# Performance work log

Measured on AMD Instinct MI355X. Metric: run time of the kernel, lower is better.

The kernel has to match this reference:

```python
import jax, jax.numpy as jnp
import numpy as np

EMB = 1024
HEADS = 16
HEAD_DIM = EMB // HEADS


def setup_inputs() -> dict:
    key = jax.random.key(0)
    ks = jax.random.split(key, 9)
    s = 1.0 / np.sqrt(EMB)
    x = jax.random.normal(ks[0], (2, 2048, EMB), dtype=jnp.float32)
    Wq = jax.random.normal(ks[1], (EMB, EMB), dtype=jnp.float32) * s
    bq = jnp.zeros((EMB,), dtype=jnp.float32)
    Wk = jax.random.normal(ks[2], (EMB, EMB), dtype=jnp.float32) * s
    bk = jnp.zeros((EMB,), dtype=jnp.float32)
    Wv = jax.random.normal(ks[3], (EMB, EMB), dtype=jnp.float32) * s
    bv = jnp.zeros((EMB,), dtype=jnp.float32)
    Wo = jax.random.normal(ks[4], (EMB, EMB), dtype=jnp.float32) * s
    bo = jnp.zeros((EMB,), dtype=jnp.float32)
    return {"x": x, "Wq": Wq, "bq": bq, "Wk": Wk, "bk": bk,
            "Wv": Wv, "bv": bv, "Wo": Wo, "bo": bo}


def reference(x, Wq, bq, Wk, bk, Wv, bv, Wo, bo):
    B, S, E = x.shape
    # torch Linear: y = x @ W.T + b
    q = x @ Wq.T + bq
    k = x @ Wk.T + bk
    v = x @ Wv.T + bv
    # [B,S,E] -> [B,H,S,D]
    q = q.reshape(B, S, HEADS, HEAD_DIM).transpose(0, 2, 1, 3)
    k = k.reshape(B, S, HEADS, HEAD_DIM).transpose(0, 2, 1, 3)
    v = v.reshape(B, S, HEADS, HEAD_DIM).transpose(0, 2, 1, 3)
    energy = jnp.einsum('bhqd,bhkd->bhqk', q, k)
    scaling = jnp.float32(E) ** 0.5  # NOTE: sqrt(emb_size), not sqrt(head_dim), as in source
    att = jax.nn.softmax(energy / scaling, axis=-1)
    out = jnp.einsum('bhqk,bhkd->bhqd', att, v)
    out = out.transpose(0, 2, 1, 3).reshape(B, S, E)
    return out @ Wo.T + bo
```

## Files before the change

kernel.cpp:

```cpp
#include <hip/hip_runtime.h>
#include <stdint.h>


typedef _Float16 half8  __attribute__((ext_vector_type(8)));
typedef _Float16 half4v __attribute__((ext_vector_type(4)));
typedef float    f32x4  __attribute__((ext_vector_type(4)));
typedef float    f32x16 __attribute__((ext_vector_type(16)));

#define GLD16(g, l) __builtin_amdgcn_global_load_lds(                         \
    (__attribute__((address_space(1))) void*)(g),                            \
    (__attribute__((address_space(3))) void*)(l), 16, 0, 0)

#define MFMA16(a, b, c) __builtin_amdgcn_mfma_f32_16x16x32_f16((a), (b), (c), 0, 0, 0)
#define MFMA32(a, b, c) __builtin_amdgcn_mfma_f32_32x32x16_f16((a), (b), (c), 0, 0, 0)

#if __has_builtin(__builtin_amdgcn_exp2f)
#define EXP2(x) __builtin_amdgcn_exp2f(x)
#else
#define EXP2(x) exp2f(x)
#endif

static __device__ inline uint32_t pk_u32(float a, float b)
{
    auto t = __builtin_amdgcn_cvt_pkrtz(a, b);
    return __builtin_bit_cast(uint32_t, t);
}

__global__ void cvt_all(const float* __restrict__ x,  const float* __restrict__ wq,
                        const float* __restrict__ wk, const float* __restrict__ wv,
                        const float* __restrict__ wo, _Float16* __restrict__ xb,
                        _Float16* __restrict__ wqkv, _Float16* __restrict__ wob)
{
    int i = blockIdx.x * blockDim.x + threadIdx.x;
    const float* src; _Float16* dst; int off;
    if (i < 1048576)      { src = x;  dst = xb;                 off = i; }
    else if (i < 1310720) { src = wq; dst = wqkv;               off = i - 1048576; }
    else if (i < 1572864) { src = wk; dst = wqkv + 1048576;     off = i - 1310720; }
    else if (i < 1835008) { src = wv; dst = wqkv + 2097152;     off = i - 1572864; }
    else                  { src = wo; dst = wob;                off = i - 1835008; }
    float4 f = ((const float4*)src)[off];
    half4v h = { (_Float16)f.x, (_Float16)f.y, (_Float16)f.z, (_Float16)f.w };
    ((half4v*)dst)[off] = h;
}

template<int BN, int MODE>
__global__ __launch_bounds__(256, MODE == 0 ? 3 : 2)
void gemm_f16(const _Float16* __restrict__ A, const _Float16* __restrict__ W,
              const float* __restrict__ b0, const float* __restrict__ b1,
              const float* __restrict__ b2, _Float16* __restrict__ o0,
              _Float16* __restrict__ o1, _Float16* __restrict__ o2,
              float* __restrict__ outf, float qscale)
{
    constexpr int NI = BN / 32;
    __shared__ _Float16 lA[128 * 64];
    __shared__ _Float16 lB[BN * 64];
    const int m0 = blockIdx.y * 128, n0 = blockIdx.x * BN;
    const int tid = threadIdx.x, lane = tid & 63, w = tid >> 6;
    const int wr = (w >> 1) * 64, wc = (w & 1) * (BN / 2);
    const int lrow = lane & 15, lk4 = lane >> 4;
    f32x4 acc[4][NI] = {};

    for (int k0 = 0; k0 < 1024; k0 += 64) {
        __syncthreads();
#pragma unroll
        for (int c = 0; c < 4; ++c) {
            int sidx = c * 256 + tid;
            int row = sidx >> 3, sl = sidx & 7;
            int gc = k0 + ((sl ^ (row & 7)) << 3);
            GLD16(A + (size_t)(m0 + row) * 1024 + gc, lA + (size_t)(c * 256 + w * 64) * 8);
        }
#pragma unroll
        for (int c = 0; c < BN / 32; ++c) {
            int sidx = c * 256 + tid;
            int row = sidx >> 3, sl = sidx & 7;
            int gc = k0 + ((sl ^ (row & 7)) << 3);
            GLD16(W + (size_t)(n0 + row) * 1024 + gc, lB + (size_t)(c * 256 + w * 64) * 8);
        }
        __syncthreads();

#pragma unroll
        for (int kd = 0; kd < 2; ++kd) {
            half8 af[4], bf[NI];
#pragma unroll
            for (int mi = 0; mi < 4; ++mi) {
                int ra = wr + mi * 16 + lrow;
                af[mi] = *(const half8*)(lA + ra * 64 + (((kd * 4 + lk4) ^ (ra & 7)) * 8));
            }
#pragma unroll
            for (int ni = 0; ni < NI; ++ni) {
                int rb = wc + ni * 16 + lrow;
                bf[ni] = *(const half8*)(lB + rb * 64 + (((kd * 4 + lk4) ^ (rb & 7)) * 8));
            }
#pragma unroll
            for (int mi = 0; mi < 4; ++mi)
#pragma unroll
                for (int ni = 0; ni < NI; ++ni)
                    acc[mi][ni] = MFMA16(af[mi], bf[ni], acc[mi][ni]);
        }
    }

    if (MODE == 0) {
        const int which = n0 >> 10;
        const float* bp = which == 0 ? b0 : which == 1 ? b1 : b2;
        const float scale = which == 0 ? qscale : 1.f;
        const int nh = n0 & 1023;
        float bcol[NI];
#pragma unroll
        for (int ni = 0; ni < NI; ++ni) bcol[ni] = bp[nh + wc + ni * 16 + lrow];
        if (which == 2) {
#pragma unroll
            for (int mi = 0; mi < 4; ++mi)
#pragma unroll
                for (int ni = 0; ni < NI; ++ni) {
                    int cg = nh + wc + ni * 16 + lrow;
                    int hh = cg >> 6, dd = cg & 63;
                    int sb = m0 + wr + mi * 16 + lk4 * 4;
                    int bb = sb >> 11, ss = sb & 2047;
                    int tile = ss >> 6, ks = (ss >> 4) & 3;
                    int hb = (ss >> 3) & 1, j0 = ss & 7;
                    int c2 = dd >> 5, l31v = dd & 31;
                    half4v pkv;
#pragma unroll
                    for (int r = 0; r < 4; ++r)
                        pkv[r] = (_Float16)(acc[mi][ni][r] + bcol[ni]);
                    size_t off = (size_t)(bb * 16 + hh) * 131072
                               + tile * 4096 + (ks * 2 + c2) * 512
                               + hb * 256 + l31v * 8 + j0;
                    *(half4v*)(o2 + off) = pkv;
                }
        } else if (which == 1) {
#pragma unroll
            for (int mi = 0; mi < 4; ++mi)
#pragma unroll
                for (int ni = 0; ni < NI; ++ni)
#pragma unroll
                    for (int r = 0; r < 4; ++r) {
                        int rg = m0 + wr + mi * 16 + lk4 * 4 + r;
                        int cg = nh + wc + ni * 16 + lrow;
                        float v = acc[mi][ni][r] + bcol[ni];
                        int bb = rg >> 11, ss = rg & 2047;
                        int hh = cg >> 6, dd = cg & 63;
                        int tile = ss >> 6, sbl = (ss >> 5) & 1, l31v = ss & 31;
                        int kd = dd >> 4, hv = (dd >> 3) & 1, jv = dd & 7;
                        size_t off = (size_t)(bb * 16 + hh) * 131072
                                   + tile * 4096 + (sbl * 4 + kd) * 512
                                   + hv * 256 + l31v * 8 + jv;
                        o1[off] = (_Float16)v;
                    }
        } else {
            _Float16* outh = o0;
#pragma unroll
            for (int mi = 0; mi < 4; ++mi)
#pragma unroll
                for (int ni = 0; ni < NI; ++ni)
#pragma unroll
                    for (int r = 0; r < 4; ++r) {
                        int rg = m0 + wr + mi * 16 + lk4 * 4 + r;
                        int cg = nh + wc + ni * 16 + lrow;
                        float v = (acc[mi][ni][r] + bcol[ni]) * scale;
                        int b = rg >> 11, s = rg & 2047, hh = cg >> 6, dd = cg & 63;
                        outh[(((size_t)b * 16 + hh) * 2048 + s) * 64 + dd] = (_Float16)v;
                    }
        }
    } else {
        float bcol[NI];
#pragma unroll
        for (int ni = 0; ni < NI; ++ni) bcol[ni] = b0[n0 + wc + ni * 16 + lrow];
#pragma unroll
        for (int mi = 0; mi < 4; ++mi)
#pragma unroll
            for (int ni = 0; ni < NI; ++ni)
#pragma unroll
                for (int r = 0; r < 4; ++r) {
                    int rg = m0 + wr + mi * 16 + lk4 * 4 + r;
                    int cg = n0 + wc + ni * 16 + lrow;
                    outf[(size_t)rg * 1024 + cg] = acc[mi][ni][r] + bcol[ni];
                }
    }
}

#define KVB 64
#define NT  32
__global__ __launch_bounds__(256, 2)
void attn(const _Float16* __restrict__ q, const _Float16* __restrict__ kf_,
          const _Float16* __restrict__ vf_, _Float16* __restrict__ ao)
{
    __shared__ _Float16 lKV[3 * 8192];
    const int bid0 = blockIdx.x;
    const int bid = (bid0 & 7) * 64 + (bid0 >> 3);
    const int bh = bid >> 4, q0 = (bid & 15) * 128;
    const int bb = bh >> 4, hh = bh & 15;
    const int tid = threadIdx.x, lane = tid & 63, w = tid >> 6;
    const int l31 = lane & 31, h = lane >> 5;
    const _Float16* qh = q + (size_t)bh * 2048 * 64;
    const _Float16* khf = kf_ + (size_t)bh * 131072;
    const _Float16* vhf = vf_ + (size_t)bh * 131072;

    half8 qf[4];
#pragma unroll
    for (int kd = 0; kd < 4; ++kd)
        qf[kd] = *(const half8*)(qh + (size_t)(q0 + w * 32 + l31) * 64
                                    + kd * 16 + h * 8);

    float l_ = 0.f;
    f32x16 o0 = {}, o1 = {};
    f32x16 eA0 = {}, eA1 = {}, eB0 = {}, eB1 = {};

    int sv = 0, sk = 1, sw = 2;

    auto STAGE = [&](int t, int bs) {
        const _Float16* ks = khf + (size_t)t * 4096;
        const _Float16* vs = vhf + (size_t)t * 4096;
        _Float16* dst = lKV + bs * 8192;
#pragma unroll
        for (int c = 0; c < 2; ++c) {
            int p = c * 256 + tid;
            GLD16(ks + (size_t)p * 8, dst + (size_t)p * 8);
            GLD16(vs + (size_t)p * 8, dst + 4096 + (size_t)p * 8);
        }
    };

    auto SOFTMAX = [&](const f32x16& ec0, const f32x16& ec1, half8 (&pa)[4]) {
#pragma unroll
        for (int f = 0; f < 2; ++f) {
            float p[16];
#pragma unroll
            for (int r = 0; r < 16; ++r) p[r] = EXP2(f == 0 ? ec0[r] : ec1[r]);
            l_ += (((p[0] + p[1]) + (p[2] + p[3])) + ((p[4] + p[5]) + (p[6] + p[7])))
                + (((p[8] + p[9]) + (p[10] + p[11])) + ((p[12] + p[13]) + (p[14] + p[15])));
#pragma unroll
            for (int bq = 0; bq < 2; ++bq) {
                uint32_t w0 = pk_u32(p[bq * 8 + 0], p[bq * 8 + 1]);
                uint32_t w1 = pk_u32(p[bq * 8 + 2], p[bq * 8 + 3]);
                uint32_t w2 = pk_u32(p[bq * 8 + 4], p[bq * 8 + 5]);
                uint32_t w3 = pk_u32(p[bq * 8 + 6], p[bq * 8 + 7]);
                asm volatile("v_permlane32_swap_b32 %0, %1" : "+v"(w0), "+v"(w2));
                asm volatile("v_permlane32_swap_b32 %0, %1" : "+v"(w1), "+v"(w3));
                union { uint32_t u[4]; half8 hv; } uu;
                uu.u[0] = w0; uu.u[1] = w1; uu.u[2] = w2; uu.u[3] = w3;
                pa[f * 2 + bq] = uu.hv;
            }
        }
    };

    auto BODY = [&](int t, f32x16& ec0, f32x16& ec1, f32x16& en0, f32x16& en1)
        __attribute__((always_inline))
    {
        asm volatile("s_waitcnt vmcnt(0)" ::: "memory");
        __builtin_amdgcn_s_barrier();
        __builtin_amdgcn_sched_barrier(0);
        if (t + 2 < NT) STAGE(t + 2, sw);

        const _Float16* Kb = lKV + sk * 8192;
        const _Float16* Vb = lKV + sv * 8192 + 4096;
        half8 kf[8], vf[8];
#pragma unroll
        for (int i = 0; i < 8; ++i)
            kf[i] = *(const half8*)(Kb + i * 512 + lane * 8);
#pragma unroll
        for (int i = 0; i < 8; ++i)
            vf[i] = *(const half8*)(Vb + i * 512 + lane * 8);

        __builtin_amdgcn_s_setprio(1);
        en0 = MFMA32(kf[0], qf[0], f32x16{});
        en1 = MFMA32(kf[4], qf[0], f32x16{});
#pragma unroll
        for (int kd = 1; kd < 4; ++kd) {
            en0 = MFMA32(kf[kd], qf[kd], en0);
            en1 = MFMA32(kf[4 + kd], qf[kd], en1);
        }
        __builtin_amdgcn_s_setprio(0);

        half8 pa[4];
        SOFTMAX(ec0, ec1, pa);

        __builtin_amdgcn_s_setprio(1);
#pragma unroll
        for (int ks = 0; ks < 4; ++ks) {
            o0 = MFMA32(pa[ks], vf[ks * 2], o0);
            o1 = MFMA32(pa[ks], vf[ks * 2 + 1], o1);
        }
        __builtin_amdgcn_s_setprio(0);

        int tmp = sv; sv = sk; sk = sw; sw = tmp;
    };

    STAGE(0, 0);
    STAGE(1, 1);
    asm volatile("s_waitcnt vmcnt(0)" ::: "memory");
    __builtin_amdgcn_s_barrier();
    {
        const _Float16* Kb = lKV;
        half8 kf[8];
#pragma unroll
        for (int i = 0; i < 8; ++i)
            kf[i] = *(const half8*)(Kb + i * 512 + lane * 8);
        eA0 = MFMA32(kf[0], qf[0], f32x16{});
        eA1 = MFMA32(kf[4], qf[0], f32x16{});
#pragma unroll
        for (int kd = 1; kd < 4; ++kd) {
            eA0 = MFMA32(kf[kd], qf[kd], eA0);
            eA1 = MFMA32(kf[4 + kd], qf[kd], eA1);
        }
    }

#pragma unroll 1
    for (int t = 0; t < 30; t += 2) {
        BODY(t,     eA0, eA1, eB0, eB1);
        BODY(t + 1, eB0, eB1, eA0, eA1);
    }
    BODY(30, eA0, eA1, eB0, eB1);

    {
        const _Float16* Vb = lKV + sv * 8192 + 4096;
        half8 vf[8];
#pragma unroll
        for (int i = 0; i < 8; ++i)
            vf[i] = *(const half8*)(Vb + i * 512 + lane * 8);
        half8 pa[4];
        SOFTMAX(eB0, eB1, pa);
#pragma unroll
        for (int ks = 0; ks < 4; ++ks) {
            o0 = MFMA32(pa[ks], vf[ks * 2], o0);
            o1 = MFMA32(pa[ks], vf[ks * 2 + 1], o1);
        }
    }

    l_ += __shfl_xor(l_, 32);
    const size_t obase = ((size_t)bb * 2048) * 1024 + hh * 64;
#pragma unroll
    for (int r = 0; r < 16; ++r) {
        int qr = (r & 3) + 8 * (r >> 2) + 4 * h;
        float linv = 1.f / __shfl(l_, qr);
        int sg = q0 + w * 32 + qr;
        ao[obase + (size_t)sg * 1024 + l31]      = (_Float16)(o0[r] * linv);
        ao[obase + (size_t)sg * 1024 + 32 + l31] = (_Float16)(o1[r] * linv);
    }
}

extern "C" void kernel_launch(void* const* d_in, const int* in_sizes, int n_in,
                              void* d_out, int out_size, void* d_ws, size_t ws_size,
                              hipStream_t stream)
{
    const float* x  = (const float*)d_in[0];
    const float* Wq = (const float*)d_in[1];
    const float* bq = (const float*)d_in[2];
    const float* Wk = (const float*)d_in[3];
    const float* bk = (const float*)d_in[4];
    const float* Wv = (const float*)d_in[5];
    const float* bv = (const float*)d_in[6];
    const float* Wo = (const float*)d_in[7];
    const float* bo = (const float*)d_in[8];
    float* out = (float*)d_out;

    char* ws = (char*)d_ws;
    _Float16* xb   = (_Float16*)(ws);
    _Float16* aob  = xb;
    _Float16* wqkv = (_Float16*)(ws + (8u  << 20));
    _Float16* wob  = (_Float16*)(ws + (14u << 20));
    _Float16* qb   = (_Float16*)(ws + (16u << 20));
    _Float16* kfb  = (_Float16*)(ws + (24u << 20));
    _Float16* vfb  = (_Float16*)(ws + (32u << 20));

    cvt_all<<<8192, 256, 0, stream>>>(x, Wq, Wk, Wv, Wo, xb, wqkv, wob);

    const float qscale = 1.4426950408889634f / 32.f;
    gemm_f16<128, 0><<<dim3(24, 32), 256, 0, stream>>>(
        xb, wqkv, bq, bk, bv, qb, kfb, vfb, nullptr, qscale);

    attn<<<512, 256, 0, stream>>>(qb, kfb, vfb, aob);

    gemm_f16<64, 1><<<dim3(16, 32), 256, 0, stream>>>(
        aob, wob, bo, nullptr, nullptr, nullptr, nullptr, nullptr, out, 1.f);
}
```

Baseline: 104.4 us.

## Load V tiles directly into registers, keep only K in shared memory

The attention kernel stops staging V through LDS. Each wave now loads its V fragments straight from global memory into two rotating register buffers, two tiles ahead, while K keeps a double-buffered LDS stage. This shrinks shared memory from 48KB to 16KB and removes the LDS reads of V, aiming to cut LDS traffic and raise occupancy. In exchange it adds 64 VGPRs of V buffers, makes every wave issue its own global loads for the same V tile, and depends on hand-counted vmcnt waits being correct.

```diff
diff --git a/kernel.cpp b/kernel.cpp
--- a/kernel.cpp
+++ b/kernel.cpp
@@ -185,7 +185,7 @@
 void attn(const _Float16* __restrict__ q, const _Float16* __restrict__ kf_,
           const _Float16* __restrict__ vf_, _Float16* __restrict__ ao)
 {
-    __shared__ _Float16 lKV[3 * 8192];
+    __shared__ _Float16 lK[2 * 4096];
     const int bid0 = blockIdx.x;
     const int bid = (bid0 & 7) * 64 + (bid0 >> 3);
     const int bh = bid >> 4, q0 = (bid & 15) * 128;
@@ -205,19 +205,22 @@
     float l_ = 0.f;
     f32x16 o0 = {}, o1 = {};
     f32x16 eA0 = {}, eA1 = {}, eB0 = {}, eB1 = {};
-
-    int sv = 0, sk = 1, sw = 2;
-
-    auto STAGE = [&](int t, int bs) {
-        const _Float16* ks = khf + (size_t)t * 4096;
-        const _Float16* vs = vhf + (size_t)t * 4096;
-        _Float16* dst = lKV + bs * 8192;
+    half8 vfA[8], vfB[8];
+
+    auto STAGEK = [&](int t) {
+        const _Float16* src = khf + (size_t)t * 4096;
+        _Float16* dst = lK + (t & 1) * 4096;
 #pragma unroll
         for (int c = 0; c < 2; ++c) {
             int p = c * 256 + tid;
-            GLD16(ks + (size_t)p * 8, dst + (size_t)p * 8);
-            GLD16(vs + (size_t)p * 8, dst + 4096 + (size_t)p * 8);
-        }
+            GLD16(src + (size_t)p * 8, dst + (size_t)p * 8);
+        }
+    };
+    auto LOADV = [&](int t, half8 (&dst)[8]) {
+        const _Float16* src = vhf + (size_t)t * 4096 + lane * 8;
+#pragma unroll
+        for (int i = 0; i < 8; ++i)
+            dst[i] = *(const half8*)(src + i * 512);
     };
 
     auto SOFTMAX = [&](const f32x16& ec0, const f32x16& ec1, half8 (&pa)[4]) {
@@ -243,23 +246,20 @@
         }
     };
 
-    auto BODY = [&](int t, f32x16& ec0, f32x16& ec1, f32x16& en0, f32x16& en1)
-        __attribute__((always_inline))
+    auto BODY = [&](int t, f32x16& ec0, f32x16& ec1, f32x16& en0, f32x16& en1,
+                    half8 (&vcur)[8]) __attribute__((always_inline))
     {
-        asm volatile("s_waitcnt vmcnt(0)" ::: "memory");
+        if (t < NT - 1) asm volatile("s_waitcnt vmcnt(8)" ::: "memory");
+        else            asm volatile("s_waitcnt vmcnt(0)" ::: "memory");
         __builtin_amdgcn_s_barrier();
         __builtin_amdgcn_sched_barrier(0);
-        if (t + 2 < NT) STAGE(t + 2, sw);
-
-        const _Float16* Kb = lKV + sk * 8192;
-        const _Float16* Vb = lKV + sv * 8192 + 4096;
-        half8 kf[8], vf[8];
+        if (t + 2 < NT) STAGEK(t + 2);
+
+        const _Float16* Kb = lK + ((t + 1) & 1) * 4096;
+        half8 kf[8];
 #pragma unroll
         for (int i = 0; i < 8; ++i)
             kf[i] = *(const half8*)(Kb + i * 512 + lane * 8);
-#pragma unroll
-        for (int i = 0; i < 8; ++i)
-            vf[i] = *(const half8*)(Vb + i * 512 + lane * 8);
 
         __builtin_amdgcn_s_setprio(1);
         en0 = MFMA32(kf[0], qf[0], f32x16{});
@@ -277,20 +277,22 @@
         __builtin_amdgcn_s_setprio(1);
 #pragma unroll
         for (int ks = 0; ks < 4; ++ks) {
-            o0 = MFMA32(pa[ks], vf[ks * 2], o0);
-            o1 = MFMA32(pa[ks], vf[ks * 2 + 1], o1);
+            o0 = MFMA32(pa[ks], vcur[ks * 2], o0);
+            o1 = MFMA32(pa[ks], vcur[ks * 2 + 1], o1);
         }
         __builtin_amdgcn_s_setprio(0);
 
-        int tmp = sv; sv = sk; sk = sw; sw = tmp;
+        if (t + 2 < NT) LOADV(t + 2, vcur);
     };
 
-    STAGE(0, 0);
-    STAGE(1, 1);
-    asm volatile("s_waitcnt vmcnt(0)" ::: "memory");
+    STAGEK(0);
+    STAGEK(1);
+    LOADV(0, vfA);
+    LOADV(1, vfB);
+    asm volatile("s_waitcnt vmcnt(18)" ::: "memory");
     __builtin_amdgcn_s_barrier();
     {
-        const _Float16* Kb = lKV;
+        const _Float16* Kb = lK;
         half8 kf[8];
 #pragma unroll
         for (int i = 0; i < 8; ++i)
@@ -306,23 +308,18 @@
 
 #pragma unroll 1
     for (int t = 0; t < 30; t += 2) {
-        BODY(t,     eA0, eA1, eB0, eB1);
-        BODY(t + 1, eB0, eB1, eA0, eA1);
-    }
-    BODY(30, eA0, eA1, eB0, eB1);
+        BODY(t,     eA0, eA1, eB0, eB1, vfA);
+        BODY(t + 1, eB0, eB1, eA0, eA1, vfB);
+    }
+    BODY(30, eA0, eA1, eB0, eB1, vfA);
 
     {
-        const _Float16* Vb = lKV + sv * 8192 + 4096;
-        half8 vf[8];
-#pragma unroll
-        for (int i = 0; i < 8; ++i)
-            vf[i] = *(const half8*)(Vb + i * 512 + lane * 8);
         half8 pa[4];
         SOFTMAX(eB0, eB1, pa);
 #pragma unroll
         for (int ks = 0; ks < 4; ++ks) {
-            o0 = MFMA32(pa[ks], vf[ks * 2], o0);
-            o1 = MFMA32(pa[ks], vf[ks * 2 + 1], o1);
+            o0 = MFMA32(pa[ks], vfB[ks * 2], o0);
+            o1 = MFMA32(pa[ks], vfB[ks * 2 + 1], o1);
         }
     }
 
```

New measurement: 107.4 us (median of 5 runs). 2.8% more time.
